# Optimization experiments

Measured on AMD Instinct MI355X. Metric: run time of the kernel, lower is better.

The kernel has to match this reference:

```python
import jax, jax.numpy as jnp
import numpy as np

E, T, IN, OUT, GS = 8, 2048, 2048, 2048, 64


def setup_inputs() -> dict:
    key = jax.random.key(0)
    k1, k2, k3, k4, k5 = jax.random.split(key, 5)
    x = jax.random.normal(k1, (T, IN), dtype=jnp.float32)
    # int4 codes in [0,16): stored unpacked as int32 for the reference
    qweight = jax.random.randint(k2, (E, IN, OUT), 0, 16, dtype=jnp.int32)
    G = IN // GS  # quant groups along the reduction dim
    scales = jax.random.uniform(k3, (E, G, OUT), jnp.float32, minval=0.005, maxval=0.02)
    zeros = jax.random.normal(k4, (E, G, OUT), jnp.float32) * 0.01
    scales_and_zeros = jnp.stack([scales, zeros], axis=-1)  # [E, G, OUT, 2]
    # tokens sorted by expert: per-expert counts are diffs of sorted cut points, sum == T
    cuts = jnp.sort(jax.random.randint(k5, (E - 1,), 0, T + 1, dtype=jnp.int32))
    bounds = jnp.concatenate([jnp.zeros((1,), jnp.int32), cuts, jnp.full((1,), T, jnp.int32)])
    tokens_per_expert = jnp.diff(bounds).astype(jnp.int32)  # [E]
    return {
        "x": x,
        "qweight": qweight,
        "scales_and_zeros": scales_and_zeros,
        "tokens_per_expert": tokens_per_expert,
        "group_size": GS,
    }


def reference(x, qweight, scales_and_zeros, tokens_per_expert, group_size):
    """Grouped (per-expert) int4 dequant + GEMM over an expert-sorted token matrix.

    Math of aten._weight_int4pack_mm per expert e over each quant group g:
        W_e[k, n] = (q_e[k, n] - 8) * scale_e[g, n] + zero_e[g, n],  g = k // group_size
        out[rows_e] = x[rows_e] @ W_e
    where rows_e is the contiguous slice given by cumsum(tokens_per_expert).
    """
    n_exp, in_f, out_f = qweight.shape
    n_tok = x.shape[0]
    G = in_f // group_size

    # dequantize all expert weights: [E, IN, OUT]
    q = qweight.reshape(n_exp, G, group_size, out_f).astype(x.dtype)
    scales = scales_and_zeros[..., 0][:, :, None, :]  # [E, G, 1, OUT]
    zeros = scales_and_zeros[..., 1][:, :, None, :]   # [E, G, 1, OUT]
    W = ((q - 8.0) * scales + zeros).reshape(n_exp, in_f, out_f)

    # expert id per token from the cumsum boundaries (tokens are expert-sorted)
    cum = jnp.cumsum(tokens_per_expert)                                # [E]
    eid = jnp.searchsorted(cum, jnp.arange(n_tok), side="right")       # [T]
    onehot = (eid[:, None] == jnp.arange(n_exp)[None, :]).astype(x.dtype)  # [T, E]

    # dispatch -> per-expert GEMM -> combine (jit-safe grouped GEMM)
    xe = jnp.einsum("te,ti->eti", onehot, x)       # [E, T, IN]
    ye = jnp.einsum("eti,eio->eto", xe, W)         # [E, T, OUT]
    out = jnp.einsum("te,eto->to", onehot, ye)     # [T, OUT]
    return out
```

## Files before the change

kernel.cpp:

```cpp
#include <hip/hip_runtime.h>
#include <hip/hip_bf16.h>

constexpr int NE  = 8;
constexpr int T   = 2048;
constexpr int IN  = 2048;
constexpr int OUT = 2048;
constexpr int GS  = 64;
constexpr int G   = IN / GS;

constexpr int BM = 128;
constexpr int BN = 64;
constexpr int BK = 64;
constexpr int NTILE = IN / BK;
constexpr int LDB = 64;
constexpr int MAXMT = T / BM + NE;

using short8  = __attribute__((ext_vector_type(8))) short;
using short4v = __attribute__((ext_vector_type(4))) short;
using floatx4 = __attribute__((ext_vector_type(4))) float;
using int4v   = __attribute__((ext_vector_type(4))) int;
using float4v = __attribute__((ext_vector_type(4))) float;

__global__ __launch_bounds__(256)
void cvt_x_bf16(const float* __restrict__ x, __hip_bfloat16* __restrict__ xb) {
    const int i = (blockIdx.x * 256 + threadIdx.x) * 4;
    const float4 v = *(const float4*)(x + i);
    union { unsigned long long u; __hip_bfloat162 h2[2]; } p;
    p.h2[0] = __float22bfloat162_rn(float2{v.x, v.y});
    p.h2[1] = __float22bfloat162_rn(float2{v.z, v.w});
    *(unsigned long long*)(xb + i) = p.u;
}

__global__ __launch_bounds__(256, 3)
void hqq_grouped_gemm(const __hip_bfloat16* __restrict__ xb,
                      const int*   __restrict__ qw,
                      const float* __restrict__ snz,
                      const int*   __restrict__ tpe,
                      float* __restrict__ out) {
    const int tid = threadIdx.x;
    const int n0  = blockIdx.x * BN;

    const int mt = blockIdx.y;
    int e = -1, b0 = 0, b1 = 0, tm = 0;
    {
        int base = 0, rem = mt;
#pragma unroll
        for (int i = 0; i < NE; ++i) {
            const int c  = tpe[i];
            const int nt = (c + BM - 1) >> 7;
            if (e < 0) {
                if (rem < nt) { e = i; b0 = base; b1 = base + c; tm = rem; }
                else rem -= nt;
            }
            base += c;
        }
    }
    if (e < 0) return;
    const int row0 = b0 + tm * BM;

    __shared__ __hip_bfloat16 Bs[2][BN][LDB];

    floatx4 acc[2][4];
#pragma unroll
    for (int i = 0; i < 2; ++i)
#pragma unroll
        for (int j = 0; j < 4; ++j)
            acc[i][j] = (floatx4){0.f, 0.f, 0.f, 0.f};

    const int n4  = (tid & 15) * 4;
    const int kq4 = (tid >> 4) * 4;
    const int wsz = (tid & 3) << 4;

    const int lane = tid & 63;
    const int wid  = tid >> 6;
    const int wm = wid * 32;
    const int lm = lane & 15;
    const int lk = (lane >> 4) * 8;
    const int rsz = ((lm >> 2) & 3) << 4;

    const int*    qbase  = qw + (size_t)e * IN * OUT + n0 + n4;
    const float2* szbase = (const float2*)snz + (size_t)e * G * OUT + n0 + n4;

    const int r0c = min(row0 + wm + lm,      b1 - 1);
    const int r1c = min(row0 + wm + 16 + lm, b1 - 1);
    const __hip_bfloat16* ap0 = xb + (size_t)r0c * IN + lk;
    const __hip_bfloat16* ap1 = xb + (size_t)r1c * IN + lk;

    int4v   qvA[4], qvB[4];
    float4v szA[2], szB[2];
    short8  afA[4], afB[4];

    auto issue_q = [&](int t, int4v (&qv)[4], float4v (&sz)[2]) {
        const int k0 = t * BK;
        const float4v* szp = (const float4v*)(szbase + (size_t)(k0 >> 6) * OUT);
        sz[0] = szp[0];
        sz[1] = szp[1];
#pragma unroll
        for (int kk = 0; kk < 4; ++kk)
            qv[kk] = *(const int4v*)(qbase + (size_t)(k0 + kq4 + kk) * OUT);
    };

    auto issue_af = [&](int t, short8 (&af)[4]) {
        const int k0 = t * BK;
        af[0] = *(const short8*)(ap0 + k0);
        af[1] = *(const short8*)(ap1 + k0);
        af[2] = *(const short8*)(ap0 + k0 + 32);
        af[3] = *(const short8*)(ap1 + k0 + 32);
    };

    auto stage = [&](__hip_bfloat16 (&B)[BN][LDB], int4v (&qv)[4], float4v (&sz)[2]) {
#pragma unroll
        for (int nn = 0; nn < 4; ++nn) {
            const float sc = sz[nn >> 1][(nn & 1) * 2];
            const float cc = sz[nn >> 1][(nn & 1) * 2 + 1] - 8.0f * sc;
            union { short4v v; __hip_bfloat162 h2[2]; } pb;
            pb.h2[0] = __float22bfloat162_rn(float2{(float)qv[0][nn] * sc + cc,
                                                    (float)qv[1][nn] * sc + cc});
            pb.h2[1] = __float22bfloat162_rn(float2{(float)qv[2][nn] * sc + cc,
                                                    (float)qv[3][nn] * sc + cc});
            *(short4v*)&B[n4 + nn][kq4 ^ wsz] = pb.v;
        }
    };

    auto mfma_tile = [&](const __hip_bfloat16 (&B)[BN][LDB], const short8 (&af)[4]) {
#pragma unroll
        for (int ks2 = 0; ks2 < 2; ++ks2) {
            short8 bfr[4];
#pragma unroll
            for (int j = 0; j < 4; ++j)
                bfr[j] = *(const short8*)&B[j * 16 + lm][(ks2 * 32 + lk) ^ rsz];
#pragma unroll
            for (int i = 0; i < 2; ++i)
#pragma unroll
                for (int j = 0; j < 4; ++j)
                    acc[i][j] = __builtin_amdgcn_mfma_f32_16x16x32_bf16(
                        af[ks2 * 2 + i], bfr[j], acc[i][j], 0, 0, 0);
        }
    };

#define TILE_SYNC()                                          \
    asm volatile("s_waitcnt lgkmcnt(0)" ::: "memory");       \
    __builtin_amdgcn_s_barrier();                            \
    __builtin_amdgcn_sched_barrier(0)

    issue_q(0, qvA, szA);
    issue_q(1, qvB, szB);
    issue_af(0, afA);
    issue_af(1, afB);

    for (int t = 0; t < NTILE; t += 2) {
        stage(Bs[0], qvA, szA);
        { const int tn = (t + 2 < NTILE) ? t + 2 : NTILE - 1; issue_q(tn, qvA, szA); }
        TILE_SYNC();
        mfma_tile(Bs[0], afA);
        { const int tn = (t + 2 < NTILE) ? t + 2 : NTILE - 1; issue_af(tn, afA); }

        stage(Bs[1], qvB, szB);
        { const int tn = (t + 3 < NTILE) ? t + 3 : NTILE - 1; issue_q(tn, qvB, szB); }
        TILE_SYNC();
        mfma_tile(Bs[1], afB);
        { const int tn = (t + 3 < NTILE) ? t + 3 : NTILE - 1; issue_af(tn, afB); }
    }
#undef TILE_SYNC

    const int lq = (lane >> 4) * 4;
#pragma unroll
    for (int i = 0; i < 2; ++i) {
#pragma unroll
        for (int r = 0; r < 4; ++r) {
            const int row = row0 + wm + i * 16 + lq + r;
            if (row < b1) {
                float* op = out + (size_t)row * OUT + n0 + lm;
#pragma unroll
                for (int j = 0; j < 4; ++j)
                    op[j * 16] = acc[i][j][r];
            }
        }
    }
}

extern "C" void kernel_launch(void* const* d_in, const int* in_sizes, int n_in,
                              void* d_out, int out_size, void* d_ws, size_t ws_size,
                              hipStream_t stream) {
    const float* x   = (const float*)d_in[0];
    const int*   qw  = (const int*)d_in[1];
    const float* snz = (const float*)d_in[2];
    const int*   tpe = (const int*)d_in[3];
    float* out = (float*)d_out;
    __hip_bfloat16* xb = (__hip_bfloat16*)d_ws;

    cvt_x_bf16<<<(T * IN) / (256 * 4), 256, 0, stream>>>(x, xb);

    dim3 grid(OUT / BN, MAXMT, 1);
    hqq_grouped_gemm<<<grid, 256, 0, stream>>>(xb, qw, snz, tpe, out);
}
```

Measured before the change: 248.0 us.

## Use inline-asm global loads with explicit vmcnt waits to pipeline tiles

Replaces compiler-generated global loads with inline-asm global_load_dwordx4 instructions and adds explicit s_waitcnt vmcnt counts before the stage and MFMA phases. This keeps prefetched weight and activation loads in flight across tile boundaries instead of letting the compiler insert conservative full waits. The main loop is peeled into an explicit phase sequence. Correctness now depends on hand-counted outstanding-load numbers. The compiler cannot see the data dependencies through the asm, so a wrong count would read registers before their loads finish.

```diff
diff --git a/kernel.cpp b/kernel.cpp
--- a/kernel.cpp
+++ b/kernel.cpp
@@ -86,26 +86,34 @@
     const __hip_bfloat16* ap0 = xb + (size_t)r0c * IN + lk;
     const __hip_bfloat16* ap1 = xb + (size_t)r1c * IN + lk;
 
-    int4v   qvA[4], qvB[4];
-    float4v szA[2], szB[2];
+    int4v   qvX[4], qvY[4];
+    float4v szX[2], szY[2];
     short8  afA[4], afB[4];
+
+#define GLOAD16(dst, addr) \
+    asm volatile("global_load_dwordx4 %0, %1, off" : "=v"(dst) : "v"(addr))
+#define GLOAD16_OFF(dst, addr, B) \
+    asm volatile("global_load_dwordx4 %0, %1, off offset:" #B : "=v"(dst) : "v"(addr))
 
     auto issue_q = [&](int t, int4v (&qv)[4], float4v (&sz)[2]) {
         const int k0 = t * BK;
         const float4v* szp = (const float4v*)(szbase + (size_t)(k0 >> 6) * OUT);
-        sz[0] = szp[0];
-        sz[1] = szp[1];
-#pragma unroll
-        for (int kk = 0; kk < 4; ++kk)
-            qv[kk] = *(const int4v*)(qbase + (size_t)(k0 + kq4 + kk) * OUT);
+        GLOAD16(sz[0], szp);
+        GLOAD16_OFF(sz[1], szp, 16);
+#pragma unroll
+        for (int kk = 0; kk < 4; ++kk) {
+            const int* qp = qbase + (size_t)(k0 + kq4 + kk) * OUT;
+            GLOAD16(qv[kk], qp);
+        }
     };
 
     auto issue_af = [&](int t, short8 (&af)[4]) {
-        const int k0 = t * BK;
-        af[0] = *(const short8*)(ap0 + k0);
-        af[1] = *(const short8*)(ap1 + k0);
-        af[2] = *(const short8*)(ap0 + k0 + 32);
-        af[3] = *(const short8*)(ap1 + k0 + 32);
+        const __hip_bfloat16* p0 = ap0 + t * BK;
+        const __hip_bfloat16* p1 = ap1 + t * BK;
+        GLOAD16(af[0], p0);
+        GLOAD16(af[1], p1);
+        GLOAD16_OFF(af[2], p0, 64);
+        GLOAD16_OFF(af[3], p1, 64);
     };
 
     auto stage = [&](__hip_bfloat16 (&B)[BN][LDB], int4v (&qv)[4], float4v (&sz)[2]) {
@@ -138,30 +146,34 @@
         }
     };
 
-#define TILE_SYNC()                                          \
-    asm volatile("s_waitcnt lgkmcnt(0)" ::: "memory");       \
-    __builtin_amdgcn_s_barrier();                            \
-    __builtin_amdgcn_sched_barrier(0)
-
-    issue_q(0, qvA, szA);
-    issue_q(1, qvB, szB);
+#define PHASE(TT, QS, AS, BB, WA, WE)                                   \
+    asm volatile("s_waitcnt vmcnt(" #WA ")" ::: "memory");              \
+    __builtin_amdgcn_sched_barrier(0);                                  \
+    stage(Bs[BB], qv##QS, sz##QS);                                      \
+    issue_q((TT) + 2 < NTILE ? (TT) + 2 : NTILE - 1, qv##QS, sz##QS);   \
+    asm volatile("s_waitcnt lgkmcnt(0)" ::: "memory");                  \
+    __builtin_amdgcn_s_barrier();                                       \
+    __builtin_amdgcn_sched_barrier(0);                                  \
+    asm volatile("s_waitcnt vmcnt(" #WE ")" ::: "memory");              \
+    __builtin_amdgcn_sched_barrier(0);                                  \
+    mfma_tile(Bs[BB], af##AS);                                          \
+    issue_af((TT) + 2 < NTILE ? (TT) + 2 : NTILE - 1, af##AS);
+
+    issue_q(0, qvX, szX);
+    issue_q(1, qvY, szY);
     issue_af(0, afA);
     issue_af(1, afB);
 
-    for (int t = 0; t < NTILE; t += 2) {
-        stage(Bs[0], qvA, szA);
-        { const int tn = (t + 2 < NTILE) ? t + 2 : NTILE - 1; issue_q(tn, qvA, szA); }
-        TILE_SYNC();
-        mfma_tile(Bs[0], afA);
-        { const int tn = (t + 2 < NTILE) ? t + 2 : NTILE - 1; issue_af(tn, afA); }
-
-        stage(Bs[1], qvB, szB);
-        { const int tn = (t + 3 < NTILE) ? t + 3 : NTILE - 1; issue_q(tn, qvB, szB); }
-        TILE_SYNC();
-        mfma_tile(Bs[1], afB);
-        { const int tn = (t + 3 < NTILE) ? t + 3 : NTILE - 1; issue_af(tn, afB); }
+    PHASE(0, X, A, 0, 14, 10)
+    PHASE(1, Y, B, 1, 18, 16)
+    for (int it = 0; it < 15; ++it) {
+        const int t = 2 + it * 2;
+        PHASE(t,     X, A, 0, 14, 16)
+        PHASE(t + 1, Y, B, 1, 14, 16)
     }
-#undef TILE_SYNC
+#undef PHASE
+#undef GLOAD16
+#undef GLOAD16_OFF
 
     const int lq = (lane >> 4) * 4;
 #pragma unroll
```

New measurement: 248.3 us. About the same (+0.1%).
